# Optimization experiments

Hardware: AMD Instinct MI355X
Metric: run time of the kernel (lower is better)

Reference implementation:

```python
import jax, jax.numpy as jnp
import numpy as np

EMB_DIM = 256
HEAD_DIM = 32


def setup_inputs() -> dict:
    key = jax.random.key(0)
    kx, kq, kk, kv = jax.random.split(key, 4)
    B, S = 4, 4096
    x = jax.random.normal(kx, (B, S, EMB_DIM), dtype=jnp.float32)
    # Linear(emb_dim, head_dim, bias=False): store as [emb_dim, head_dim]
    sc = 1.0 / np.sqrt(EMB_DIM)
    Wq = jax.random.normal(kq, (EMB_DIM, HEAD_DIM), dtype=jnp.float32) * sc
    Wk = jax.random.normal(kk, (EMB_DIM, HEAD_DIM), dtype=jnp.float32) * sc
    Wv = jax.random.normal(kv, (EMB_DIM, HEAD_DIM), dtype=jnp.float32) * sc
    return {"x": x, "Wq": Wq, "Wk": Wk, "Wv": Wv}


def reference(x, Wq, Wk, Wv):
    # single-head attention with POST-softmax scaling (as in source).
    # Dropout treated as identity (eval mode) for determinism.
    scaling = HEAD_DIM ** (-0.5)
    q = jnp.einsum('bse,ed->bsd', x, Wq)
    k = jnp.einsum('bse,ed->bsd', x, Wk)
    v = jnp.einsum('bse,ed->bsd', x, Wv)
    energy = jnp.einsum('bqd,bkd->bqk', q, k)  # [B,S,S]
    att = jax.nn.softmax(energy, axis=-1) * scaling
    out = jnp.einsum('bqk,bkd->bqd', att, v)
    return out
```

## Files before the change

### kernel.cpp

```cpp
#include <hip/hip_runtime.h>

#define EMB 256
#define HD 32
#define SEQ 4096
#define NSPLIT 8
#define KRANGE 512
#define NT (KRANGE / 32)
#define NQROW 16384

typedef _Float16 half8 __attribute__((ext_vector_type(8)));
typedef _Float16 half4v __attribute__((ext_vector_type(4)));
typedef _Float16 half2v __attribute__((ext_vector_type(2)));
typedef float floatx4 __attribute__((ext_vector_type(4)));
typedef float floatx16 __attribute__((ext_vector_type(16)));
typedef unsigned uint2v __attribute__((ext_vector_type(2)));

#define L2E 1.44269504088896340736f
#define SCALING 0.17677669529663687f
#define DEFER_THR 8.0f

__device__ __forceinline__ half8 mk8(unsigned a, unsigned b, unsigned c, unsigned d) {
  union { unsigned u[4]; half8 h; } z;
  z.u[0] = a; z.u[1] = b; z.u[2] = c; z.u[3] = d;
  return z.h;
}

__device__ __forceinline__ void plswap(unsigned& a, unsigned& b) {
#if __has_builtin(__builtin_amdgcn_permlane32_swap)
  uint2v r = __builtin_amdgcn_permlane32_swap(a, b, false, false);
  a = r[0]; b = r[1];
#else
  unsigned sa = (unsigned)__shfl_xor((int)a, 32);
  unsigned sb = (unsigned)__shfl_xor((int)b, 32);
  bool hi = (threadIdx.x & 32) != 0;
  unsigned na = hi ? sb : a;
  unsigned nb = hi ? b : sa;
  a = na; b = nb;
#endif
}

__device__ __forceinline__ float sum2(unsigned pk, float acc) {
  half2v a = __builtin_bit_cast(half2v, pk);
#if __has_builtin(__builtin_amdgcn_fdot2)
  half2v one; one[0] = (_Float16)1.f; one[1] = (_Float16)1.f;
  return __builtin_amdgcn_fdot2(a, one, acc, false);
#else
  return acc + (float)a[0] + (float)a[1];
#endif
}

__global__ __launch_bounds__(256) void qkv_kernel(const float* __restrict__ x,
                                                  const float* __restrict__ Wq,
                                                  const float* __restrict__ Wk,
                                                  const float* __restrict__ Wv,
                                                  _Float16* __restrict__ qw,
                                                  _Float16* __restrict__ kw,
                                                  _Float16* __restrict__ vt2) {
  __shared__ _Float16 wsl[24576];
  const int tid = threadIdx.x;

#pragma unroll
  for (int i = 0; i < 24; ++i) {
    const float* W = (i < 8) ? Wq : ((i < 16) ? Wk : Wv);
    int lu = (i & 7) * 1024 + tid * 4;
    float4 v4 = *(const float4*)(W + lu);
    int e = lu >> 5;
    int d0 = lu & 31;
    int kc = e >> 5, quad = (e >> 3) & 3, j = e & 7;
    int half = d0 >> 4;
    int n0 = d0 & 15;
    int mat = i >> 3;
    int base = (((mat * 2 + half) * 8 + kc) << 9) + (quad << 7) + j;
    float sc = (i < 8) ? L2E : 1.f;
    wsl[base + (n0 + 0) * 8] = (_Float16)(v4.x * sc);
    wsl[base + (n0 + 1) * 8] = (_Float16)(v4.y * sc);
    wsl[base + (n0 + 2) * 8] = (_Float16)(v4.z * sc);
    wsl[base + (n0 + 3) * 8] = (_Float16)(v4.w * sc);
  }
  __syncthreads();

  int lane = tid & 63, wave = tid >> 6;
  int n = lane & 15, quad = lane >> 4;
  int rowbase = blockIdx.x * 64 + wave * 16;

  floatx4 cq0 = {0,0,0,0}, cq1 = {0,0,0,0};
  floatx4 ck0 = {0,0,0,0}, ck1 = {0,0,0,0};
  floatx4 cv0 = {0,0,0,0}, cv1 = {0,0,0,0};

#pragma unroll
  for (int kc = 0; kc < 8; ++kc) {
    const float* xp = x + (size_t)(rowbase + n) * EMB + kc * 32 + quad * 8;
    float4 xa = *(const float4*)(xp);
    float4 xb = *(const float4*)(xp + 4);
    half8 a;
    a[0] = (_Float16)xa.x; a[1] = (_Float16)xa.y; a[2] = (_Float16)xa.z; a[3] = (_Float16)xa.w;
    a[4] = (_Float16)xb.x; a[5] = (_Float16)xb.y; a[6] = (_Float16)xb.z; a[7] = (_Float16)xb.w;
    const _Float16* wp = wsl + (kc << 9) + (lane << 3);
    half8 bq0 = *(const half8*)(wp);
    half8 bq1 = *(const half8*)(wp + (8  << 9));
    half8 bk0 = *(const half8*)(wp + (16 << 9));
    half8 bk1 = *(const half8*)(wp + (24 << 9));
    half8 bv0 = *(const half8*)(wp + (32 << 9));
    half8 bv1 = *(const half8*)(wp + (40 << 9));
    cq0 = __builtin_amdgcn_mfma_f32_16x16x32_f16(a, bq0, cq0, 0, 0, 0);
    cq1 = __builtin_amdgcn_mfma_f32_16x16x32_f16(a, bq1, cq1, 0, 0, 0);
    ck0 = __builtin_amdgcn_mfma_f32_16x16x32_f16(a, bk0, ck0, 0, 0, 0);
    ck1 = __builtin_amdgcn_mfma_f32_16x16x32_f16(a, bk1, ck1, 0, 0, 0);
    cv0 = __builtin_amdgcn_mfma_f32_16x16x32_f16(a, bv0, cv0, 0, 0, 0);
    cv1 = __builtin_amdgcn_mfma_f32_16x16x32_f16(a, bv1, cv1, 0, 0, 0);
  }

  int b = rowbase >> 12;
  int s0 = rowbase & (SEQ - 1);
  _Float16* vbase = vt2 + (size_t)b * SEQ * HD;
#pragma unroll
  for (int r = 0; r < 4; ++r) {
    int row = rowbase + quad * 4 + r;
    qw[row * HD + n]      = (_Float16)cq0[r];
    qw[row * HD + n + 16] = (_Float16)cq1[r];
    kw[row * HD + n]      = (_Float16)ck0[r];
    kw[row * HD + n + 16] = (_Float16)ck1[r];
    int s = s0 + quad * 4 + r;
    int blk = (s >> 3) << 8, sl = s & 7;
    vbase[blk + n * 8 + sl]        = (_Float16)cv0[r];
    vbase[blk + (n + 16) * 8 + sl] = (_Float16)cv1[r];
  }
}

__global__ __launch_bounds__(512, 4) void attn_kernel(const _Float16* __restrict__ q,
                                                      const _Float16* __restrict__ k,
                                                      const _Float16* __restrict__ vt2,
                                                      float* __restrict__ out) {
  __shared__ float sO[NSPLIT * 32 * 36];
  __shared__ float sM[NSPLIT * 32];
  __shared__ float sL[NSPLIT * 32];

  const int t = threadIdx.x;
  const int w = t >> 6, lane = t & 63;
  const int n2 = lane & 31, h = lane >> 5;
  const int qrow0 = blockIdx.x * 32;
  const int b = qrow0 >> 12;
  const int key0 = w * KRANGE;

  const _Float16* kb = k   + (size_t)(b * SEQ + key0) * HD;
  const _Float16* vb = vt2 + (size_t)b * SEQ * HD + (size_t)key0 * HD;

  half8 qf0 = *(const half8*)(q + (qrow0 + n2) * HD + h * 8);
  half8 qf1 = *(const half8*)(q + (qrow0 + n2) * HD + 16 + h * 8);

  floatx16 o;
#pragma unroll
  for (int r = 0; r < 16; ++r) o[r] = 0.f;
  const floatx16 zero16 = o;
  float m = -__builtin_huge_valf();
  float mtrue = -__builtin_huge_valf();
  float l = 0.f;

  auto ldt = [&](int tile, half8& k0, half8& k1, half8& v0, half8& v1) {
    const _Float16* kn = kb + (size_t)(tile * 32 + n2) * HD;
    const _Float16* vn = vb + tile * 1024;
    k0 = *(const half8*)(kn + h * 8);
    k1 = *(const half8*)(kn + 16 + h * 8);
    v0 = *(const half8*)(vn + h * 256 + n2 * 8);
    v1 = *(const half8*)(vn + 512 + h * 256 + n2 * 8);
  };

  auto tilecomp = [&](half8 tka0, half8 tka1, half8 tva0, half8 tva1) {
    floatx16 s = __builtin_amdgcn_mfma_f32_32x32x16_f16(tka0, qf0, zero16, 0, 0, 0);
    s = __builtin_amdgcn_mfma_f32_32x32x16_f16(tka1, qf1, s, 0, 0, 0);

    floatx4 s0 = {s[0], s[1], s[2], s[3]};
    floatx4 s1 = {s[4], s[5], s[6], s[7]};
    floatx4 s2 = {s[8], s[9], s[10], s[11]};
    floatx4 s3 = {s[12], s[13], s[14], s[15]};
    floatx4 t01 = __builtin_elementwise_max(s0, s1);
    floatx4 t23 = __builtin_elementwise_max(s2, s3);
    floatx4 t4  = __builtin_elementwise_max(t01, t23);
    float mm = fmaxf(fmaxf(t4[0], t4[1]), fmaxf(t4[2], t4[3]));
    mm = fmaxf(mm, __shfl_xor(mm, 32));
    mtrue = fmaxf(mtrue, mm);

    if (__any(mm > m + DEFER_THR)) {
      float mnew = fmaxf(m, mm);
      float alpha = __builtin_amdgcn_exp2f(m - mnew);
      m = mnew;
#pragma unroll
      for (int r = 0; r < 16; ++r) o[r] *= alpha;
      l *= alpha;
    }

    unsigned pk[8];
#pragma unroll
    for (int g = 0; g < 8; ++g) {
      float p0 = __builtin_amdgcn_exp2f(s[2 * g] - m);
      float p1 = __builtin_amdgcn_exp2f(s[2 * g + 1] - m);
      pk[g] = __builtin_bit_cast(unsigned, __builtin_amdgcn_cvt_pkrtz(p0, p1));
    }

    float lA = sum2(pk[3], sum2(pk[2], sum2(pk[1], sum2(pk[0], 0.f))));
    float lB = sum2(pk[7], sum2(pk[6], sum2(pk[5], sum2(pk[4], 0.f))));
    l += lA + lB;

    unsigned b00 = pk[0], b02 = pk[2]; plswap(b00, b02);
    unsigned b01 = pk[1], b03 = pk[3]; plswap(b01, b03);
    unsigned b10 = pk[4], b12 = pk[6]; plswap(b10, b12);
    unsigned b11 = pk[5], b13 = pk[7]; plswap(b11, b13);

    o = __builtin_amdgcn_mfma_f32_32x32x16_f16(tva0, mk8(b00, b01, b02, b03), o, 0, 0, 0);
    o = __builtin_amdgcn_mfma_f32_32x32x16_f16(tva1, mk8(b10, b11, b12, b13), o, 0, 0, 0);
  };

  half8 ak0, ak1, av0, av1, bk0, bk1, bv0, bv1;
  ldt(0, ak0, ak1, av0, av1);
  ldt(1, bk0, bk1, bv0, bv1);

#pragma unroll
  for (int kt = 0; kt < NT; kt += 2) {
    half8 ck0, ck1, cv0, cv1, dk0, dk1, dv0, dv1;
    ldt((kt + 2) & (NT - 1), ck0, ck1, cv0, cv1);
    tilecomp(ak0, ak1, av0, av1);
    ldt((kt + 3) & (NT - 1), dk0, dk1, dv0, dv1);
    tilecomp(bk0, bk1, bv0, bv1);
    ak0 = ck0; ak1 = ck1; av0 = cv0; av1 = cv1;
    bk0 = dk0; bk1 = dk1; bv0 = dv0; bv1 = dv1;
  }

  float scale = __builtin_amdgcn_exp2f(m - mtrue);
  l *= scale;
  l = l + __shfl_xor(l, 32);

#pragma unroll
  for (int bb = 0; bb < 4; ++bb) {
    floatx4 pv = {o[4 * bb + 0] * scale, o[4 * bb + 1] * scale,
                  o[4 * bb + 2] * scale, o[4 * bb + 3] * scale};
    *(floatx4*)&sO[w * 1152 + n2 * 36 + 8 * bb + 4 * h] = pv;
  }
  if (h == 0) {
    sM[w * 32 + n2] = mtrue;
    sL[w * 32 + n2] = l;
  }
  __syncthreads();

#pragma unroll
  for (int it = 0; it < 2; ++it) {
    int idx = it * 512 + t;
    int qr = idx >> 5, d = idx & 31;
    float mv[NSPLIT];
    float ms = -__builtin_huge_valf();
#pragma unroll
    for (int w2 = 0; w2 < NSPLIT; ++w2) {
      mv[w2] = sM[w2 * 32 + qr];
      ms = fmaxf(ms, mv[w2]);
    }
    float L = 0.f, O = 0.f;
#pragma unroll
    for (int w2 = 0; w2 < NSPLIT; ++w2) {
      float ww = __builtin_amdgcn_exp2f(mv[w2] - ms);
      L += ww * sL[w2 * 32 + qr];
      O += ww * sO[w2 * 1152 + qr * 36 + d];
    }
    out[(size_t)(qrow0 + qr) * HD + d] = O * SCALING / L;
  }
}

extern "C" void kernel_launch(void* const* d_in, const int* in_sizes, int n_in,
                              void* d_out, int out_size, void* d_ws, size_t ws_size,
                              hipStream_t stream) {
  const float* x  = (const float*)d_in[0];
  const float* Wq = (const float*)d_in[1];
  const float* Wk = (const float*)d_in[2];
  const float* Wv = (const float*)d_in[3];
  float* out = (float*)d_out;

  _Float16* qw  = (_Float16*)d_ws;
  _Float16* kw  = qw + NQROW * HD;
  _Float16* vt2 = kw + NQROW * HD;

  qkv_kernel<<<256, 256, 0, stream>>>(x, Wq, Wk, Wv, qw, kw, vt2);
  attn_kernel<<<512, 512, 0, stream>>>(qw, kw, vt2, out);
}
```

Measured before the change: 93.20 us.

## Split QKV projection across three times more blocks and raise attention occupancy hint

The projection kernel now launches one block per (matrix, row group), so each block stages and multiplies only one weight matrix. This triples the grid from 256 to 768 blocks and cuts shared memory per block, giving better coverage of the CUs. The cost is that each x tile is read from global memory three times instead of once. The attention kernel's launch bounds min-blocks hint goes from 4 to 8, which can push the compiler to limit registers and may cause spills.

```diff
diff --git a/kernel.cpp b/kernel.cpp
--- a/kernel.cpp
+++ b/kernel.cpp
@@ -56,22 +56,24 @@
                                                   _Float16* __restrict__ qw,
                                                   _Float16* __restrict__ kw,
                                                   _Float16* __restrict__ vt2) {
-  __shared__ _Float16 wsl[24576];
+  __shared__ _Float16 wsl[8192];
   const int tid = threadIdx.x;
-
-#pragma unroll
-  for (int i = 0; i < 24; ++i) {
-    const float* W = (i < 8) ? Wq : ((i < 16) ? Wk : Wv);
-    int lu = (i & 7) * 1024 + tid * 4;
+  const int mat = blockIdx.x >> 8;
+  const int rg  = blockIdx.x & 255;
+
+  const float* W = (mat == 0) ? Wq : ((mat == 1) ? Wk : Wv);
+  const float sc = (mat == 0) ? L2E : 1.f;
+
+#pragma unroll
+  for (int i = 0; i < 8; ++i) {
+    int lu = i * 1024 + tid * 4;
     float4 v4 = *(const float4*)(W + lu);
     int e = lu >> 5;
     int d0 = lu & 31;
     int kc = e >> 5, quad = (e >> 3) & 3, j = e & 7;
     int half = d0 >> 4;
     int n0 = d0 & 15;
-    int mat = i >> 3;
-    int base = (((mat * 2 + half) * 8 + kc) << 9) + (quad << 7) + j;
-    float sc = (i < 8) ? L2E : 1.f;
+    int base = ((half * 8 + kc) << 9) + (quad << 7) + j;
     wsl[base + (n0 + 0) * 8] = (_Float16)(v4.x * sc);
     wsl[base + (n0 + 1) * 8] = (_Float16)(v4.y * sc);
     wsl[base + (n0 + 2) * 8] = (_Float16)(v4.z * sc);
@@ -81,11 +83,9 @@
 
   int lane = tid & 63, wave = tid >> 6;
   int n = lane & 15, quad = lane >> 4;
-  int rowbase = blockIdx.x * 64 + wave * 16;
-
-  floatx4 cq0 = {0,0,0,0}, cq1 = {0,0,0,0};
-  floatx4 ck0 = {0,0,0,0}, ck1 = {0,0,0,0};
-  floatx4 cv0 = {0,0,0,0}, cv1 = {0,0,0,0};
+  int rowbase = rg * 64 + wave * 16;
+
+  floatx4 c0 = {0,0,0,0}, c1 = {0,0,0,0};
 
 #pragma unroll
   for (int kc = 0; kc < 8; ++kc) {
@@ -95,39 +95,35 @@
     half8 a;
     a[0] = (_Float16)xa.x; a[1] = (_Float16)xa.y; a[2] = (_Float16)xa.z; a[3] = (_Float16)xa.w;
     a[4] = (_Float16)xb.x; a[5] = (_Float16)xb.y; a[6] = (_Float16)xb.z; a[7] = (_Float16)xb.w;
-    const _Float16* wp = wsl + (kc << 9) + (lane << 3);
-    half8 bq0 = *(const half8*)(wp);
-    half8 bq1 = *(const half8*)(wp + (8  << 9));
-    half8 bk0 = *(const half8*)(wp + (16 << 9));
-    half8 bk1 = *(const half8*)(wp + (24 << 9));
-    half8 bv0 = *(const half8*)(wp + (32 << 9));
-    half8 bv1 = *(const half8*)(wp + (40 << 9));
-    cq0 = __builtin_amdgcn_mfma_f32_16x16x32_f16(a, bq0, cq0, 0, 0, 0);
-    cq1 = __builtin_amdgcn_mfma_f32_16x16x32_f16(a, bq1, cq1, 0, 0, 0);
-    ck0 = __builtin_amdgcn_mfma_f32_16x16x32_f16(a, bk0, ck0, 0, 0, 0);
-    ck1 = __builtin_amdgcn_mfma_f32_16x16x32_f16(a, bk1, ck1, 0, 0, 0);
-    cv0 = __builtin_amdgcn_mfma_f32_16x16x32_f16(a, bv0, cv0, 0, 0, 0);
-    cv1 = __builtin_amdgcn_mfma_f32_16x16x32_f16(a, bv1, cv1, 0, 0, 0);
-  }
-
-  int b = rowbase >> 12;
-  int s0 = rowbase & (SEQ - 1);
-  _Float16* vbase = vt2 + (size_t)b * SEQ * HD;
-#pragma unroll
-  for (int r = 0; r < 4; ++r) {
-    int row = rowbase + quad * 4 + r;
-    qw[row * HD + n]      = (_Float16)cq0[r];
-    qw[row * HD + n + 16] = (_Float16)cq1[r];
-    kw[row * HD + n]      = (_Float16)ck0[r];
-    kw[row * HD + n + 16] = (_Float16)ck1[r];
-    int s = s0 + quad * 4 + r;
-    int blk = (s >> 3) << 8, sl = s & 7;
-    vbase[blk + n * 8 + sl]        = (_Float16)cv0[r];
-    vbase[blk + (n + 16) * 8 + sl] = (_Float16)cv1[r];
-  }
-}
-
-__global__ __launch_bounds__(512, 4) void attn_kernel(const _Float16* __restrict__ q,
+    half8 b0 = *(const half8*)(wsl + (kc << 9) + (lane << 3));
+    half8 b1 = *(const half8*)(wsl + ((8 + kc) << 9) + (lane << 3));
+    c0 = __builtin_amdgcn_mfma_f32_16x16x32_f16(a, b0, c0, 0, 0, 0);
+    c1 = __builtin_amdgcn_mfma_f32_16x16x32_f16(a, b1, c1, 0, 0, 0);
+  }
+
+  if (mat == 2) {
+    int b = rowbase >> 12;
+    int s0 = rowbase & (SEQ - 1);
+    _Float16* vb = vt2 + (size_t)b * SEQ * HD;
+#pragma unroll
+    for (int r = 0; r < 4; ++r) {
+      int s = s0 + quad * 4 + r;
+      int blk = (s >> 3) << 8, sl = s & 7;
+      vb[blk + n * 8 + sl]        = (_Float16)c0[r];
+      vb[blk + (n + 16) * 8 + sl] = (_Float16)c1[r];
+    }
+  } else {
+    _Float16* dst = (mat == 0) ? qw : kw;
+#pragma unroll
+    for (int r = 0; r < 4; ++r) {
+      int row = rowbase + quad * 4 + r;
+      dst[row * HD + n]      = (_Float16)c0[r];
+      dst[row * HD + n + 16] = (_Float16)c1[r];
+    }
+  }
+}
+
+__global__ __launch_bounds__(512, 8) void attn_kernel(const _Float16* __restrict__ q,
                                                       const _Float16* __restrict__ k,
                                                       const _Float16* __restrict__ vt2,
                                                       float* __restrict__ out) {
@@ -276,6 +272,6 @@
   _Float16* kw  = qw + NQROW * HD;
   _Float16* vt2 = kw + NQROW * HD;
 
-  qkv_kernel<<<256, 256, 0, stream>>>(x, Wq, Wk, Wv, qw, kw, vt2);
+  qkv_kernel<<<768, 256, 0, stream>>>(x, Wq, Wk, Wv, qw, kw, vt2);
   attn_kernel<<<512, 512, 0, stream>>>(qw, kw, vt2, out);
 }
```

Result: slower. 153.6 us (+64.8%).
